# Kernel tuning notes

Measured on AMD Instinct MI355X. Metric: run time of the kernel, lower is better.

The kernel has to match this reference:

```python
import jax, jax.numpy as jnp
import numpy as np

N, E, D, L, B, T = 50000, 600000, 128, 7, 512, 10
ATOM_DIMS = [119, 4, 12, 12, 10, 6, 6, 2, 2]
BOND_DIMS = [5, 6, 2]
MSG_EPS = 1e-7   # GENConv message epsilon
BN_EPS = 1e-5    # torch BatchNorm1d eps


def _offsets(dims):
    return jnp.asarray(np.concatenate([[0], np.cumsum(dims[:-1])]), dtype=jnp.int32)


def setup_inputs():
    key = jax.random.key(0)
    k = lambda i: jax.random.fold_in(key, i)
    x = jnp.stack([jax.random.randint(k(i), (N,), 0, d) for i, d in enumerate(ATOM_DIMS)], axis=1)
    edge_attr = jnp.stack([jax.random.randint(k(100 + i), (E,), 0, d) for i, d in enumerate(BOND_DIMS)], axis=1)
    edge_index = jax.random.randint(k(200), (2, E), 0, N)
    batch = jnp.sort(jax.random.randint(k(201), (N,), 0, B))
    atom_table = 0.1 * jax.random.normal(k(300), (sum(ATOM_DIMS), D), jnp.float32)
    bond_table = 0.1 * jax.random.normal(k(301), (sum(BOND_DIMS), D), jnp.float32)
    norm_gamma = jnp.ones((L, D), jnp.float32)
    norm_beta = jnp.zeros((L, D), jnp.float32)
    t = 0.1 * jnp.ones((L,), jnp.float32)
    mlp_w1 = 0.05 * jax.random.normal(k(302), (L, D, 2 * D), jnp.float32)
    mlp_b1 = jnp.zeros((L, 2 * D), jnp.float32)
    mlp_bng = jnp.ones((L, 2 * D), jnp.float32)
    mlp_bnb = jnp.zeros((L, 2 * D), jnp.float32)
    mlp_w2 = 0.05 * jax.random.normal(k(303), (L, 2 * D, D), jnp.float32)
    mlp_b2 = jnp.zeros((L, D), jnp.float32)
    pred_w = 0.05 * jax.random.normal(k(304), (D, T), jnp.float32)
    pred_b = jnp.zeros((T,), jnp.float32)
    return dict(x=x, edge_index=edge_index, edge_attr=edge_attr, batch=batch,
                atom_offsets=_offsets(ATOM_DIMS), bond_offsets=_offsets(BOND_DIMS),
                atom_table=atom_table, bond_table=bond_table,
                norm_gamma=norm_gamma, norm_beta=norm_beta, t=t,
                mlp_w1=mlp_w1, mlp_b1=mlp_b1, mlp_bng=mlp_bng, mlp_bnb=mlp_bnb,
                mlp_w2=mlp_w2, mlp_b2=mlp_b2, pred_w=pred_w, pred_b=pred_b)


def _batchnorm(z, gamma, beta):
    # training-mode BatchNorm1d: batch stats, biased variance
    mu = z.mean(0)
    var = z.var(0)
    return (z - mu) * jax.lax.rsqrt(var + BN_EPS) * gamma + beta


def _genconv(h, ea, src, dst, t, w1, b1, g1, bt1, w2, b2):
    # GENConv: message = relu(x_j + edge_attr) + eps; softmax aggregation with temperature t
    msg = jax.nn.relu(h[src] + ea) + MSG_EPS                 # [E, D]
    logits = msg * t
    m = jax.ops.segment_max(logits, dst, num_segments=N)     # [N, D]
    m = jax.lax.stop_gradient(jnp.where(jnp.isfinite(m), m, 0.0))
    e = jnp.exp(logits - m[dst])
    denom = jax.ops.segment_sum(e, dst, num_segments=N)
    alpha = e / (denom[dst] + 1e-16)
    aggr = jax.ops.segment_sum(msg * alpha, dst, num_segments=N)  # [N, D]
    out = h + aggr                                           # update: x_r + aggr
    z = _batchnorm(out @ w1 + b1, g1, bt1)                   # MLP: D -> 2D (BN, ReLU) -> D
    return jax.nn.relu(z) @ w2 + b2


def reference(x, edge_index, edge_attr, batch, atom_offsets, bond_offsets,
              atom_table, bond_table, norm_gamma, norm_beta, t,
              mlp_w1, mlp_b1, mlp_bng, mlp_bnb, mlp_w2, mlp_b2, pred_w, pred_b):
    h = atom_table[x + atom_offsets[None, :]].sum(1)               # [N, D] AtomEncoder
    ea = bond_table[edge_attr + bond_offsets[None, :]].sum(1)      # [E, D] BondEncoder
    src, dst = edge_index[0], edge_index[1]
    # first layer: bare conv
    h = _genconv(h, ea, src, dst, t[0], mlp_w1[0], mlp_b1[0], mlp_bng[0], mlp_bnb[0], mlp_w2[0], mlp_b2[0])
    # remaining layers: res+ blocks (norm -> act -> conv -> residual); dropout=0
    for i in range(1, L):
        r = jax.nn.relu(_batchnorm(h, norm_gamma[i], norm_beta[i]))
        r = _genconv(r, ea, src, dst, t[i], mlp_w1[i], mlp_b1[i], mlp_bng[i], mlp_bnb[i], mlp_w2[i], mlp_b2[i])
        h = h + r
    h = _batchnorm(h, norm_gamma[0], norm_beta[0])                 # layers[0].norm
    # global mean pool over graphs
    sums = jax.ops.segment_sum(h, batch, num_segments=B)
    cnts = jax.ops.segment_sum(jnp.ones((N,), h.dtype), batch, num_segments=B)
    graph_emb = sums / jnp.maximum(cnts, 1.0)[:, None]
    return graph_emb @ pred_w + pred_b                             # [B, T]
```

## Files before the change

### kernel.cpp

```cpp
#include <hip/hip_runtime.h>
#include <hip/hip_bf16.h>

#define N_NODES 50000
#define N_EDGES 600000
#define D 128
#define D2 256
#define NGRAPH 512
#define NTARGET 10
#define NSB 49
#define NSLOT 32

static constexpr float MSG_EPS_F = 1e-7f;
static constexpr float BN_EPS_F  = 1e-5f;

typedef _Float16 half8 __attribute__((ext_vector_type(8)));
typedef _Float16 half4v __attribute__((ext_vector_type(4)));
typedef float f32x4 __attribute__((ext_vector_type(4)));
#define MFMA16(a, b, c) __builtin_amdgcn_mfma_f32_16x16x32_f16(a, b, c, 0, 0, 0)

__global__ __launch_bounds__(256) void k_encode(
    const int* __restrict__ x, const int* __restrict__ aoff,
    const float* __restrict__ atab, float* __restrict__ h,
    _Float16* __restrict__ rh, int* __restrict__ deg) {
  int tid = blockIdx.x * 256 + threadIdx.x;
  if (tid < N_NODES) deg[tid] = 0;
  int n = tid >> 5, f4 = (tid & 31) << 2;
  if (n >= N_NODES) return;
  float4 acc = make_float4(0.f, 0.f, 0.f, 0.f);
#pragma unroll
  for (int i = 0; i < 9; ++i) {
    int row = x[n * 9 + i] + aoff[i];
    float4 v = *(const float4*)&atab[row * D + f4];
    acc.x += v.x; acc.y += v.y; acc.z += v.z; acc.w += v.w;
  }
  *(float4*)&h[(size_t)n * D + f4] = acc;
  half4v o = {(_Float16)acc.x, (_Float16)acc.y, (_Float16)acc.z, (_Float16)acc.w};
  *(half4v*)&rh[(size_t)n * D + f4] = o;
}

__global__ __launch_bounds__(128) void k_combo(
    const int* __restrict__ boff, const float* __restrict__ btab,
    float* __restrict__ combo) {
  int c = blockIdx.x, t = threadIdx.x;
  int a0 = c / 12, a1 = (c % 12) / 2, a2 = c % 2;
  combo[c * D + t] = btab[(boff[0] + a0) * D + t] +
                     btab[(boff[1] + a1) * D + t] +
                     btab[(boff[2] + a2) * D + t];
}

__global__ __launch_bounds__(256) void k_packW(
    const float* __restrict__ w1, const float* __restrict__ w2,
    _Float16* __restrict__ w1p, _Float16* __restrict__ w2p) {
  int t = blockIdx.x * 256 + threadIdx.x;
  if (t < 7 * 4096) {
    int lane = t & 63, ntAll = (t >> 6) & 15, kc = (t >> 10) & 3, l = t >> 12;
    int q = lane >> 4, c = ntAll * 16 + (lane & 15);
    int kbase = kc * 32 + q * 8;
    const float* W = w1 + (size_t)l * D * D2;
    half8 v;
#pragma unroll
    for (int j = 0; j < 8; ++j) v[j] = (_Float16)W[(size_t)(kbase + j) * D2 + c];
    *(half8*)&w1p[(size_t)t * 8] = v;
  } else {
    int u = t - 7 * 4096;
    if (u < 7 * 4096) {
      int lane = u & 63, nt = (u >> 6) & 7, kcAll = (u >> 9) & 7, l = u >> 12;
      int q = lane >> 4, c = nt * 16 + (lane & 15);
      int kbase = kcAll * 32 + q * 8;
      const float* W = w2 + (size_t)l * D2 * D;
      half8 v;
#pragma unroll
      for (int j = 0; j < 8; ++j) v[j] = (_Float16)W[(size_t)(kbase + j) * D + c];
      *(half8*)&w2p[(size_t)u * 8] = v;
    }
  }
}

__global__ __launch_bounds__(256) void k_degree(
    const int* __restrict__ ei, int* __restrict__ deg) {
  int e = blockIdx.x * 256 + threadIdx.x;
  if (e >= N_EDGES) return;
  atomicAdd(&deg[ei[N_EDGES + e]], 1);
}

__global__ __launch_bounds__(1024) void k_scan1(
    const int* __restrict__ deg, int* __restrict__ excl, int* __restrict__ bsum) {
  __shared__ int tmp[1024];
  int t = threadIdx.x, i = blockIdx.x * 1024 + t;
  int v = (i < N_NODES) ? deg[i] : 0;
  tmp[t] = v;
  __syncthreads();
  for (int off = 1; off < 1024; off <<= 1) {
    int add = (t >= off) ? tmp[t - off] : 0;
    __syncthreads();
    tmp[t] += add;
    __syncthreads();
  }
  if (i < N_NODES) excl[i] = tmp[t] - v;
  if (t == 1023) bsum[blockIdx.x] = tmp[1023];
}

__global__ __launch_bounds__(64) void k_scan2(int* __restrict__ bsum) {
  __shared__ int s[64];
  int t = threadIdx.x;
  int v = (t < NSB) ? bsum[t] : 0;
  s[t] = v;
  __syncthreads();
  for (int off = 1; off < 64; off <<= 1) {
    int add = (t >= off) ? s[t - off] : 0;
    __syncthreads();
    s[t] += add;
    __syncthreads();
  }
  if (t < NSB) bsum[t] = s[t] - v;
}

__global__ __launch_bounds__(256) void k_scan3(
    const int* __restrict__ excl, const int* __restrict__ bsum,
    int* __restrict__ rowptr, int* __restrict__ cursor) {
  int i = blockIdx.x * 256 + threadIdx.x;
  if (i < N_NODES) {
    int v = excl[i] + bsum[i >> 10];
    rowptr[i] = v;
    cursor[i] = v;
  }
  if (i == N_NODES) rowptr[N_NODES] = N_EDGES;
}

__global__ __launch_bounds__(256) void k_scatter(
    const int* __restrict__ ei, const int* __restrict__ eattr,
    int* __restrict__ cursor, int* __restrict__ payload) {
  int e = blockIdx.x * 256 + threadIdx.x;
  if (e >= N_EDGES) return;
  int src = ei[e], dst = ei[N_EDGES + e];
  int cid = eattr[e * 3 + 0] * 12 + eattr[e * 3 + 1] * 2 + eattr[e * 3 + 2];
  int pos = atomicAdd(&cursor[dst], 1);
  payload[pos] = (src << 6) | cid;
}

__global__ __launch_bounds__(256) void k_gbounds(
    const int* __restrict__ batch, int* __restrict__ gstart) {
  int n = blockIdx.x * 256 + threadIdx.x;
  if (n >= N_NODES) return;
  int b0 = batch[n];
  int b1 = (n + 1 < N_NODES) ? batch[n + 1] : NGRAPH;
  for (int bb = b0 + 1; bb <= b1; ++bb) gstart[bb] = n + 1;
  if (n == 0)
    for (int bb = 0; bb <= b0; ++bb) gstart[bb] = 0;
}

__global__ __launch_bounds__(256) void k_prenorm(
    const float* __restrict__ h, const float* __restrict__ statHs,
    const float* __restrict__ gamma, const float* __restrict__ beta,
    _Float16* __restrict__ rh) {
  __shared__ float sH[256];
  int t = threadIdx.x;
  {
    float a = 0.f;
#pragma unroll
    for (int s = 0; s < NSLOT; ++s) a += statHs[s * 256 + t];
    sH[t] = a;
  }
  __syncthreads();
  int tid = blockIdx.x * 256 + t;
  int n = tid >> 5, f4 = (t & 31) << 2;
  if (n >= N_NODES) return;
  const float invN = 1.0f / (float)N_NODES;
  float4 s  = *(const float4*)&sH[f4];
  float4 sq = *(const float4*)&sH[D + f4];
  float4 g  = *(const float4*)&gamma[f4];
  float4 b  = *(const float4*)&beta[f4];
  float4 hv = *(const float4*)&h[(size_t)n * D + f4];
  float mu = s.x * invN, var = sq.x * invN - mu * mu;
  float ox = fmaxf((hv.x - mu) * rsqrtf(var + BN_EPS_F) * g.x + b.x, 0.f);
  mu = s.y * invN; var = sq.y * invN - mu * mu;
  float oy = fmaxf((hv.y - mu) * rsqrtf(var + BN_EPS_F) * g.y + b.y, 0.f);
  mu = s.z * invN; var = sq.z * invN - mu * mu;
  float oz = fmaxf((hv.z - mu) * rsqrtf(var + BN_EPS_F) * g.z + b.z, 0.f);
  mu = s.w * invN; var = sq.w * invN - mu * mu;
  float ow = fmaxf((hv.w - mu) * rsqrtf(var + BN_EPS_F) * g.w + b.w, 0.f);
  half4v o = {(_Float16)ox, (_Float16)oy, (_Float16)oz, (_Float16)ow};
  *(half4v*)&rh[(size_t)n * D + f4] = o;
}

__global__ __launch_bounds__(256) void k_aggr(
    const _Float16* __restrict__ rh, const int* __restrict__ rowptr,
    const int* __restrict__ payload, const float* __restrict__ combo,
    const float* __restrict__ tptr, int l, _Float16* __restrict__ aggrh,
    float* __restrict__ stat1s, float* __restrict__ statHs) {
  if (blockIdx.x < NSLOT) {
    float* z1 = stat1s + blockIdx.x * 512;
    float* zH = statHs + blockIdx.x * 256;
    for (int j = threadIdx.x; j < 768; j += 256) {
      if (j < 512) z1[j] = 0.f;
      else zH[j - 512] = 0.f;
    }
  }
  int tid = blockIdx.x * 256 + threadIdx.x;
  int dst = tid >> 5, f4 = (tid & 31) << 2;
  if (dst >= N_NODES) return;
  float tv = tptr[l];
  int s = rowptr[dst], e = rowptr[dst + 1];
  float4 den = make_float4(0.f, 0.f, 0.f, 0.f);
  float4 S = make_float4(0.f, 0.f, 0.f, 0.f);
  int i = s;
  for (; i + 1 < e; i += 2) {
    int p0 = payload[i], p1 = payload[i + 1];
    half4v r0 = *(const half4v*)&rh[(size_t)(p0 >> 6) * D + f4];
    half4v r1 = *(const half4v*)&rh[(size_t)(p1 >> 6) * D + f4];
    float4 cv0 = *(const float4*)&combo[(p0 & 63) * D + f4];
    float4 cv1 = *(const float4*)&combo[(p1 & 63) * D + f4];
    float m0x = fmaxf((float)r0[0] + cv0.x, 0.f) + MSG_EPS_F;
    float m0y = fmaxf((float)r0[1] + cv0.y, 0.f) + MSG_EPS_F;
    float m0z = fmaxf((float)r0[2] + cv0.z, 0.f) + MSG_EPS_F;
    float m0w = fmaxf((float)r0[3] + cv0.w, 0.f) + MSG_EPS_F;
    float m1x = fmaxf((float)r1[0] + cv1.x, 0.f) + MSG_EPS_F;
    float m1y = fmaxf((float)r1[1] + cv1.y, 0.f) + MSG_EPS_F;
    float m1z = fmaxf((float)r1[2] + cv1.z, 0.f) + MSG_EPS_F;
    float m1w = fmaxf((float)r1[3] + cv1.w, 0.f) + MSG_EPS_F;
    float e0x = __expf(m0x * tv), e0y = __expf(m0y * tv);
    float e0z = __expf(m0z * tv), e0w = __expf(m0w * tv);
    float e1x = __expf(m1x * tv), e1y = __expf(m1y * tv);
    float e1z = __expf(m1z * tv), e1w = __expf(m1w * tv);
    den.x += e0x + e1x; den.y += e0y + e1y;
    den.z += e0z + e1z; den.w += e0w + e1w;
    S.x += m0x * e0x + m1x * e1x; S.y += m0y * e0y + m1y * e1y;
    S.z += m0z * e0z + m1z * e1z; S.w += m0w * e0w + m1w * e1w;
  }
  if (i < e) {
    int p0 = payload[i];
    half4v r0 = *(const half4v*)&rh[(size_t)(p0 >> 6) * D + f4];
    float4 cv0 = *(const float4*)&combo[(p0 & 63) * D + f4];
    float m0x = fmaxf((float)r0[0] + cv0.x, 0.f) + MSG_EPS_F;
    float m0y = fmaxf((float)r0[1] + cv0.y, 0.f) + MSG_EPS_F;
    float m0z = fmaxf((float)r0[2] + cv0.z, 0.f) + MSG_EPS_F;
    float m0w = fmaxf((float)r0[3] + cv0.w, 0.f) + MSG_EPS_F;
    float e0x = __expf(m0x * tv), e0y = __expf(m0y * tv);
    float e0z = __expf(m0z * tv), e0w = __expf(m0w * tv);
    den.x += e0x; den.y += e0y; den.z += e0z; den.w += e0w;
    S.x += m0x * e0x; S.y += m0y * e0y; S.z += m0z * e0z; S.w += m0w * e0w;
  }
  half4v o;
  o[0] = (_Float16)(S.x / (den.x + 1e-16f));
  o[1] = (_Float16)(S.y / (den.y + 1e-16f));
  o[2] = (_Float16)(S.z / (den.z + 1e-16f));
  o[3] = (_Float16)(S.w / (den.w + 1e-16f));
  *(half4v*)&aggrh[(size_t)dst * D + f4] = o;
}

__global__ __launch_bounds__(256) void k_gemm1(
    const _Float16* __restrict__ rh, const _Float16* __restrict__ aggrh,
    const _Float16* __restrict__ w1p, const float* __restrict__ b1,
    _Float16* __restrict__ z1h, float* __restrict__ stat1s) {
  __shared__ __align__(16) _Float16 Af[512 * 8];
  int tid = threadIdx.x;
  int row0 = blockIdx.x * 32;
  int slot = blockIdx.x & (NSLOT - 1);

#pragma unroll
  for (int s0 = 0; s0 < 2; ++s0) {
    int s = s0 * 256 + tid;
    int kc = s >> 7, mt = (s >> 6) & 1, l2 = s & 63;
    int row = row0 + mt * 16 + (l2 & 15);
    int kb = kc * 32 + ((l2 >> 4) << 3);
    half8 v;
    if (row < N_NODES) {
      half8 rv = *(const half8*)&rh[(size_t)row * D + kb];
      half8 av = *(const half8*)&aggrh[(size_t)row * D + kb];
      v = rv + av;
    } else {
#pragma unroll
      for (int j = 0; j < 8; ++j) v[j] = (_Float16)0.f;
    }
    *(half8*)&Af[s * 8] = v;
  }
  __syncthreads();

  int wv = tid >> 6, ln = tid & 63;
  f32x4 acc[2][4];
#pragma unroll
  for (int i = 0; i < 2; ++i)
#pragma unroll
    for (int j = 0; j < 4; ++j) acc[i][j] = (f32x4){0.f, 0.f, 0.f, 0.f};

#pragma unroll
  for (int kc = 0; kc < 4; ++kc) {
    half8 a0 = *(half8*)&Af[((kc * 2 + 0) * 64 + ln) * 8];
    half8 a1 = *(half8*)&Af[((kc * 2 + 1) * 64 + ln) * 8];
#pragma unroll
    for (int nt = 0; nt < 4; ++nt) {
      int ntAll = wv * 4 + nt;
      half8 b = *(const half8*)&w1p[((size_t)(kc * 16 + ntAll) * 64 + ln) * 8];
      acc[0][nt] = MFMA16(a0, b, acc[0][nt]);
      acc[1][nt] = MFMA16(a1, b, acc[1][nt]);
    }
  }
  int lq = ln >> 4, lc = ln & 15;
  float cs[4], cq[4];
#pragma unroll
  for (int nt = 0; nt < 4; ++nt) { cs[nt] = 0.f; cq[nt] = 0.f; }
#pragma unroll
  for (int nt = 0; nt < 4; ++nt) {
    int col = (wv * 4 + nt) * 16 + lc;
    float bias = b1[col];
#pragma unroll
    for (int mt = 0; mt < 2; ++mt) {
      int rbase = row0 + mt * 16 + lq * 4;
#pragma unroll
      for (int rg = 0; rg < 4; ++rg) {
        int row = rbase + rg;
        if (row < N_NODES) {
          float z = acc[mt][nt][rg] + bias;
          z1h[(size_t)row * D2 + col] = (_Float16)z;
          cs[nt] += z; cq[nt] += z * z;
        }
      }
    }
  }
#pragma unroll
  for (int nt = 0; nt < 4; ++nt) {
    float v = cs[nt], q = cq[nt];
    v += __shfl_xor(v, 16); v += __shfl_xor(v, 32);
    q += __shfl_xor(q, 16); q += __shfl_xor(q, 32);
    if (lq == 0) {
      int col = (wv * 4 + nt) * 16 + lc;
      atomicAdd(&stat1s[slot * 512 + col], v);
      atomicAdd(&stat1s[slot * 512 + 256 + col], q);
    }
  }
}

__global__ __launch_bounds__(256) void k_gemm2(
    const _Float16* __restrict__ z1h, const float* __restrict__ stat1s,
    const float* __restrict__ g1, const float* __restrict__ bt1,
    const _Float16* __restrict__ w2p, const float* __restrict__ b2,
    float* __restrict__ h, int residual, float* __restrict__ statHs) {
  __shared__ __align__(16) _Float16 Af[1024 * 8];
  __shared__ float s1[512];
  const float invN = 1.0f / (float)N_NODES;
  int tid = threadIdx.x;
  int row0 = blockIdx.x * 32;
  int slot = blockIdx.x & (NSLOT - 1);

#pragma unroll
  for (int jj = 0; jj < 2; ++jj) {
    int j = jj * 256 + tid;
    float a = 0.f;
#pragma unroll
    for (int s = 0; s < NSLOT; ++s) a += stat1s[s * 512 + j];
    s1[j] = a;
  }
  __syncthreads();

#pragma unroll
  for (int s0 = 0; s0 < 4; ++s0) {
    int s = s0 * 256 + tid;
    int kcAll = s >> 7, mt = (s >> 6) & 1, l2 = s & 63;
    int row = row0 + mt * 16 + (l2 & 15);
    int kb = kcAll * 32 + ((l2 >> 4) << 3);
    half8 v;
    if (row < N_NODES) {
      half8 z = *(const half8*)&z1h[(size_t)row * D2 + kb];
#pragma unroll
      for (int j = 0; j < 8; ++j) {
        float mu = s1[kb + j] * invN;
        float isg = rsqrtf(s1[256 + kb + j] * invN - mu * mu + BN_EPS_F) * g1[kb + j];
        v[j] = (_Float16)fmaxf(((float)z[j] - mu) * isg + bt1[kb + j], 0.f);
      }
    } else {
#pragma unroll
      for (int j = 0; j < 8; ++j) v[j] = (_Float16)0.f;
    }
    *(half8*)&Af[s * 8] = v;
  }
  __syncthreads();

  int wv = tid >> 6, ln = tid & 63;
  f32x4 acc[2][2];
#pragma unroll
  for (int i = 0; i < 2; ++i)
#pragma unroll
    for (int j = 0; j < 2; ++j) acc[i][j] = (f32x4){0.f, 0.f, 0.f, 0.f};

#pragma unroll
  for (int kcAll = 0; kcAll < 8; ++kcAll) {
    half8 a0 = *(half8*)&Af[((kcAll * 2 + 0) * 64 + ln) * 8];
    half8 a1 = *(half8*)&Af[((kcAll * 2 + 1) * 64 + ln) * 8];
#pragma unroll
    for (int nt = 0; nt < 2; ++nt) {
      half8 b = *(const half8*)&w2p[((size_t)(kcAll * 8 + wv * 2 + nt) * 64 + ln) * 8];
      acc[0][nt] = MFMA16(a0, b, acc[0][nt]);
      acc[1][nt] = MFMA16(a1, b, acc[1][nt]);
    }
  }
  int lq = ln >> 4, lc = ln & 15;
  float cs[2], cq[2];
#pragma unroll
  for (int nt = 0; nt < 2; ++nt) { cs[nt] = 0.f; cq[nt] = 0.f; }
#pragma unroll
  for (int nt = 0; nt < 2; ++nt) {
    int col = (wv * 2 + nt) * 16 + lc;
    float bias = b2[col];
#pragma unroll
    for (int mt = 0; mt < 2; ++mt) {
      int rbase = row0 + mt * 16 + lq * 4;
#pragma unroll
      for (int rg = 0; rg < 4; ++rg) {
        int row = rbase + rg;
        if (row < N_NODES) {
          float v = acc[mt][nt][rg] + bias;
          if (residual) v += h[(size_t)row * D + col];
          h[(size_t)row * D + col] = v;
          cs[nt] += v; cq[nt] += v * v;
        }
      }
    }
  }
#pragma unroll
  for (int nt = 0; nt < 2; ++nt) {
    float v = cs[nt], q = cq[nt];
    v += __shfl_xor(v, 16); v += __shfl_xor(v, 32);
    q += __shfl_xor(q, 16); q += __shfl_xor(q, 32);
    if (lq == 0) {
      int col = (wv * 2 + nt) * 16 + lc;
      atomicAdd(&statHs[slot * 256 + col], v);
      atomicAdd(&statHs[slot * 256 + 128 + col], q);
    }
  }
}

__global__ __launch_bounds__(256) void k_pool(
    const float* __restrict__ h, const int* __restrict__ gstart,
    float* __restrict__ psum) {
  __shared__ float4 red[256];
  int b = blockIdx.x, tid = threadIdx.x;
  int fl = (tid & 31) << 2, ns = tid >> 5;
  int gs = gstart[b], ge = gstart[b + 1];
  float4 acc = make_float4(0.f, 0.f, 0.f, 0.f);
  for (int n = gs + ns; n < ge; n += 8) {
    float4 v = *(const float4*)&h[(size_t)n * D + fl];
    acc.x += v.x; acc.y += v.y; acc.z += v.z; acc.w += v.w;
  }
  red[tid] = acc;
  __syncthreads();
  if (ns < 4) {
    float4 o = red[tid + 128];
    acc.x += o.x; acc.y += o.y; acc.z += o.z; acc.w += o.w;
    red[tid] = acc;
  }
  __syncthreads();
  if (ns < 2) {
    float4 o = red[tid + 64];
    acc.x += o.x; acc.y += o.y; acc.z += o.z; acc.w += o.w;
    red[tid] = acc;
  }
  __syncthreads();
  if (ns == 0) {
    float4 o = red[tid + 32];
    acc.x += o.x; acc.y += o.y; acc.z += o.z; acc.w += o.w;
    *(float4*)&psum[(size_t)b * D + fl] = acc;
  }
}

__global__ __launch_bounds__(64) void k_pred(
    const float* __restrict__ psum, const int* __restrict__ gstart,
    const float* __restrict__ statHs, const float* __restrict__ gamma,
    const float* __restrict__ beta, const float* __restrict__ pw,
    const float* __restrict__ pb, float* __restrict__ out) {
  __shared__ float sH[256];
  int b = blockIdx.x, t = threadIdx.x;
  for (int j = t; j < 256; j += 64) {
    float a = 0.f;
#pragma unroll
    for (int s = 0; s < NSLOT; ++s) a += statHs[s * 256 + j];
    sH[j] = a;
  }
  __syncthreads();
  if (t >= NTARGET) return;
  int gs = gstart[b], ge = gstart[b + 1];
  float acc = pb[t];
  if (ge > gs) {
    const float invN = 1.0f / (float)N_NODES;
    float inv = 1.0f / (float)(ge - gs);
    for (int k = 0; k < D; ++k) {
      float mu = sH[k] * invN;
      float var = sH[D + k] * invN - mu * mu;
      float emb = (psum[(size_t)b * D + k] * inv - mu) * rsqrtf(var + BN_EPS_F) * gamma[k] + beta[k];
      acc += emb * pw[k * NTARGET + t];
    }
  }
  out[b * NTARGET + t] = acc;
}

extern "C" void kernel_launch(void* const* d_in, const int* in_sizes, int n_in,
                              void* d_out, int out_size, void* d_ws, size_t ws_size,
                              hipStream_t stream) {
  const int* x      = (const int*)d_in[0];
  const int* ei     = (const int*)d_in[1];
  const int* eattr  = (const int*)d_in[2];
  const int* batch  = (const int*)d_in[3];
  const int* aoff   = (const int*)d_in[4];
  const int* boff   = (const int*)d_in[5];
  const float* atab = (const float*)d_in[6];
  const float* btab = (const float*)d_in[7];
  const float* ngam = (const float*)d_in[8];
  const float* nbet = (const float*)d_in[9];
  const float* tptr = (const float*)d_in[10];
  const float* w1   = (const float*)d_in[11];
  const float* b1   = (const float*)d_in[12];
  const float* bng  = (const float*)d_in[13];
  const float* bnb  = (const float*)d_in[14];
  const float* w2   = (const float*)d_in[15];
  const float* b2   = (const float*)d_in[16];
  const float* pw   = (const float*)d_in[17];
  const float* pb   = (const float*)d_in[18];
  float* out = (float*)d_out;

  float* ws = (float*)d_ws;
  const size_t ND = (size_t)N_NODES * D;
  float* h      = ws;
  _Float16* rh  = (_Float16*)(ws + 1 * ND);
  _Float16* aggrh = (_Float16*)(ws + 1 * ND + ND / 2);
  _Float16* z1h = (_Float16*)(ws + 2 * ND);
  float* stat1s = ws + 3 * ND;
  float* statHs = stat1s + NSLOT * 512;
  float* psum   = statHs + NSLOT * 256;
  float* combo  = psum + (size_t)NGRAPH * D;
  _Float16* w1p = (_Float16*)(combo + 60 * D);
  _Float16* w2p = w1p + 7 * 32768;
  int* ibuf     = (int*)(w2p + 7 * 32768);
  int* rowptr   = ibuf;
  int* cursor   = rowptr + N_NODES + 1;
  int* deg      = cursor + N_NODES;
  int* payload  = deg + N_NODES;
  int* gstart   = payload + N_EDGES;
  int* excl     = gstart + NGRAPH + 1;
  int* bsum     = excl + N_NODES;

  const int nodeBlocks = (N_NODES * 32 + 255) / 256;
  const int edgeThreadBlocks = (N_EDGES + 255) / 256;
  const int nBlocks256 = (N_NODES + 255) / 256;
  const int gRows32 = (N_NODES + 31) / 32;

  k_encode<<<nodeBlocks, 256, 0, stream>>>(x, aoff, atab, h, rh, deg);
  k_combo<<<60, 128, 0, stream>>>(boff, btab, combo);
  k_packW<<<(2 * 7 * 4096 + 255) / 256, 256, 0, stream>>>(w1, w2, w1p, w2p);
  k_gbounds<<<nBlocks256, 256, 0, stream>>>(batch, gstart);
  k_degree<<<edgeThreadBlocks, 256, 0, stream>>>(ei, deg);
  k_scan1<<<NSB, 1024, 0, stream>>>(deg, excl, bsum);
  k_scan2<<<1, 64, 0, stream>>>(bsum);
  k_scan3<<<(N_NODES + 256) / 256, 256, 0, stream>>>(excl, bsum, rowptr, cursor);
  k_scatter<<<edgeThreadBlocks, 256, 0, stream>>>(ei, eattr, cursor, payload);

  for (int l = 0; l < 7; ++l) {
    if (l > 0)
      k_prenorm<<<nodeBlocks, 256, 0, stream>>>(h, statHs, ngam + l * D, nbet + l * D, rh);
    k_aggr<<<nodeBlocks, 256, 0, stream>>>(rh, rowptr, payload, combo, tptr, l, aggrh,
                                           stat1s, statHs);
    k_gemm1<<<gRows32, 256, 0, stream>>>(rh, aggrh, w1p + (size_t)l * 32768,
                                         b1 + l * D2, z1h, stat1s);
    k_gemm2<<<gRows32, 256, 0, stream>>>(z1h, stat1s, bng + l * D2, bnb + l * D2,
                                         w2p + (size_t)l * 32768, b2 + l * D,
                                         h, l > 0 ? 1 : 0, statHs);
  }

  k_pool<<<NGRAPH, 256, 0, stream>>>(h, gstart, psum);
  k_pred<<<NGRAPH, 64, 0, stream>>>(psum, gstart, statHs, ngam, nbet, pw, pb, out);
}
```

Measured before the change: 909.3 us.

## Widen aggregation lanes, store combo in fp16, fuse residual add and pool/pred

The aggregation kernel now gives each thread 8 features through half8 loads, using 16 threads per node instead of 32, and reads the bond-combo table in fp16. It adds the node's own features to the aggregate before writing, so gemm1 reads one fp16 input instead of two. The pool and prediction kernels are merged into one launch. Together these cut gather bandwidth, gemm1 input traffic and launch count, at the price of fp16 rounding of the combo table and fewer threads per node in aggregation.

```diff
diff --git a/kernel.cpp b/kernel.cpp
--- a/kernel.cpp
+++ b/kernel.cpp
@@ -40,12 +40,12 @@
 
 __global__ __launch_bounds__(128) void k_combo(
     const int* __restrict__ boff, const float* __restrict__ btab,
-    float* __restrict__ combo) {
+    _Float16* __restrict__ comboh) {
   int c = blockIdx.x, t = threadIdx.x;
   int a0 = c / 12, a1 = (c % 12) / 2, a2 = c % 2;
-  combo[c * D + t] = btab[(boff[0] + a0) * D + t] +
-                     btab[(boff[1] + a1) * D + t] +
-                     btab[(boff[2] + a2) * D + t];
+  comboh[c * D + t] = (_Float16)(btab[(boff[0] + a0) * D + t] +
+                                 btab[(boff[1] + a1) * D + t] +
+                                 btab[(boff[2] + a2) * D + t]);
 }
 
 __global__ __launch_bounds__(256) void k_packW(
@@ -185,8 +185,8 @@
 
 __global__ __launch_bounds__(256) void k_aggr(
     const _Float16* __restrict__ rh, const int* __restrict__ rowptr,
-    const int* __restrict__ payload, const float* __restrict__ combo,
-    const float* __restrict__ tptr, int l, _Float16* __restrict__ aggrh,
+    const int* __restrict__ payload, const _Float16* __restrict__ comboh,
+    const float* __restrict__ tptr, int l, _Float16* __restrict__ xh,
     float* __restrict__ stat1s, float* __restrict__ statHs) {
   if (blockIdx.x < NSLOT) {
     float* z1 = stat1s + blockIdx.x * 512;
@@ -197,61 +197,53 @@
     }
   }
   int tid = blockIdx.x * 256 + threadIdx.x;
-  int dst = tid >> 5, f4 = (tid & 31) << 2;
+  int dst = tid >> 4, f8 = (tid & 15) << 3;
   if (dst >= N_NODES) return;
   float tv = tptr[l];
   int s = rowptr[dst], e = rowptr[dst + 1];
-  float4 den = make_float4(0.f, 0.f, 0.f, 0.f);
-  float4 S = make_float4(0.f, 0.f, 0.f, 0.f);
+  float den[8], S[8];
+#pragma unroll
+  for (int j = 0; j < 8; ++j) { den[j] = 0.f; S[j] = 0.f; }
   int i = s;
   for (; i + 1 < e; i += 2) {
     int p0 = payload[i], p1 = payload[i + 1];
-    half4v r0 = *(const half4v*)&rh[(size_t)(p0 >> 6) * D + f4];
-    half4v r1 = *(const half4v*)&rh[(size_t)(p1 >> 6) * D + f4];
-    float4 cv0 = *(const float4*)&combo[(p0 & 63) * D + f4];
-    float4 cv1 = *(const float4*)&combo[(p1 & 63) * D + f4];
-    float m0x = fmaxf((float)r0[0] + cv0.x, 0.f) + MSG_EPS_F;
-    float m0y = fmaxf((float)r0[1] + cv0.y, 0.f) + MSG_EPS_F;
-    float m0z = fmaxf((float)r0[2] + cv0.z, 0.f) + MSG_EPS_F;
-    float m0w = fmaxf((float)r0[3] + cv0.w, 0.f) + MSG_EPS_F;
-    float m1x = fmaxf((float)r1[0] + cv1.x, 0.f) + MSG_EPS_F;
-    float m1y = fmaxf((float)r1[1] + cv1.y, 0.f) + MSG_EPS_F;
-    float m1z = fmaxf((float)r1[2] + cv1.z, 0.f) + MSG_EPS_F;
-    float m1w = fmaxf((float)r1[3] + cv1.w, 0.f) + MSG_EPS_F;
-    float e0x = __expf(m0x * tv), e0y = __expf(m0y * tv);
-    float e0z = __expf(m0z * tv), e0w = __expf(m0w * tv);
-    float e1x = __expf(m1x * tv), e1y = __expf(m1y * tv);
-    float e1z = __expf(m1z * tv), e1w = __expf(m1w * tv);
-    den.x += e0x + e1x; den.y += e0y + e1y;
-    den.z += e0z + e1z; den.w += e0w + e1w;
-    S.x += m0x * e0x + m1x * e1x; S.y += m0y * e0y + m1y * e1y;
-    S.z += m0z * e0z + m1z * e1z; S.w += m0w * e0w + m1w * e1w;
+    half8 r0 = *(const half8*)&rh[(size_t)(p0 >> 6) * D + f8];
+    half8 r1 = *(const half8*)&rh[(size_t)(p1 >> 6) * D + f8];
+    half8 c0 = *(const half8*)&comboh[(p0 & 63) * D + f8];
+    half8 c1 = *(const half8*)&comboh[(p1 & 63) * D + f8];
+#pragma unroll
+    for (int j = 0; j < 8; ++j) {
+      float m0 = fmaxf((float)r0[j] + (float)c0[j], 0.f) + MSG_EPS_F;
+      float m1 = fmaxf((float)r1[j] + (float)c1[j], 0.f) + MSG_EPS_F;
+      float e0 = __expf(m0 * tv), e1 = __expf(m1 * tv);
+      den[j] += e0 + e1;
+      S[j] += m0 * e0 + m1 * e1;
+    }
   }
   if (i < e) {
     int p0 = payload[i];
-    half4v r0 = *(const half4v*)&rh[(size_t)(p0 >> 6) * D + f4];
-    float4 cv0 = *(const float4*)&combo[(p0 & 63) * D + f4];
-    float m0x = fmaxf((float)r0[0] + cv0.x, 0.f) + MSG_EPS_F;
-    float m0y = fmaxf((float)r0[1] + cv0.y, 0.f) + MSG_EPS_F;
-    float m0z = fmaxf((float)r0[2] + cv0.z, 0.f) + MSG_EPS_F;
-    float m0w = fmaxf((float)r0[3] + cv0.w, 0.f) + MSG_EPS_F;
-    float e0x = __expf(m0x * tv), e0y = __expf(m0y * tv);
-    float e0z = __expf(m0z * tv), e0w = __expf(m0w * tv);
-    den.x += e0x; den.y += e0y; den.z += e0z; den.w += e0w;
-    S.x += m0x * e0x; S.y += m0y * e0y; S.z += m0z * e0z; S.w += m0w * e0w;
-  }
-  half4v o;
-  o[0] = (_Float16)(S.x / (den.x + 1e-16f));
-  o[1] = (_Float16)(S.y / (den.y + 1e-16f));
-  o[2] = (_Float16)(S.z / (den.z + 1e-16f));
-  o[3] = (_Float16)(S.w / (den.w + 1e-16f));
-  *(half4v*)&aggrh[(size_t)dst * D + f4] = o;
+    half8 r0 = *(const half8*)&rh[(size_t)(p0 >> 6) * D + f8];
+    half8 c0 = *(const half8*)&comboh[(p0 & 63) * D + f8];
+#pragma unroll
+    for (int j = 0; j < 8; ++j) {
+      float m0 = fmaxf((float)r0[j] + (float)c0[j], 0.f) + MSG_EPS_F;
+      float e0 = __expf(m0 * tv);
+      den[j] += e0;
+      S[j] += m0 * e0;
+    }
+  }
+  half8 ro = *(const half8*)&rh[(size_t)dst * D + f8];
+  half8 o;
+#pragma unroll
+  for (int j = 0; j < 8; ++j)
+    o[j] = (_Float16)((float)ro[j] + S[j] / (den[j] + 1e-16f));
+  *(half8*)&xh[(size_t)dst * D + f8] = o;
 }
 
 __global__ __launch_bounds__(256) void k_gemm1(
-    const _Float16* __restrict__ rh, const _Float16* __restrict__ aggrh,
-    const _Float16* __restrict__ w1p, const float* __restrict__ b1,
-    _Float16* __restrict__ z1h, float* __restrict__ stat1s) {
+    const _Float16* __restrict__ xh, const _Float16* __restrict__ w1p,
+    const float* __restrict__ b1, _Float16* __restrict__ z1h,
+    float* __restrict__ stat1s) {
   __shared__ __align__(16) _Float16 Af[512 * 8];
   int tid = threadIdx.x;
   int row0 = blockIdx.x * 32;
@@ -265,9 +257,7 @@
     int kb = kc * 32 + ((l2 >> 4) << 3);
     half8 v;
     if (row < N_NODES) {
-      half8 rv = *(const half8*)&rh[(size_t)row * D + kb];
-      half8 av = *(const half8*)&aggrh[(size_t)row * D + kb];
-      v = rv + av;
+      v = *(const half8*)&xh[(size_t)row * D + kb];
     } else {
 #pragma unroll
       for (int j = 0; j < 8; ++j) v[j] = (_Float16)0.f;
@@ -429,11 +419,21 @@
   }
 }
 
-__global__ __launch_bounds__(256) void k_pool(
+__global__ __launch_bounds__(256) void k_poolpred(
     const float* __restrict__ h, const int* __restrict__ gstart,
-    float* __restrict__ psum) {
+    const float* __restrict__ statHs, const float* __restrict__ gamma,
+    const float* __restrict__ beta, const float* __restrict__ pw,
+    const float* __restrict__ pb, float* __restrict__ out) {
+  __shared__ float sH[256];
+  __shared__ float emb[128];
   __shared__ float4 red[256];
   int b = blockIdx.x, tid = threadIdx.x;
+  {
+    float a = 0.f;
+#pragma unroll
+    for (int s = 0; s < NSLOT; ++s) a += statHs[s * 256 + tid];
+    sH[tid] = a;
+  }
   int fl = (tid & 31) << 2, ns = tid >> 5;
   int gs = gstart[b], ge = gstart[b + 1];
   float4 acc = make_float4(0.f, 0.f, 0.f, 0.f);
@@ -458,38 +458,25 @@
   if (ns == 0) {
     float4 o = red[tid + 32];
     acc.x += o.x; acc.y += o.y; acc.z += o.z; acc.w += o.w;
-    *(float4*)&psum[(size_t)b * D + fl] = acc;
-  }
-}
-
-__global__ __launch_bounds__(64) void k_pred(
-    const float* __restrict__ psum, const int* __restrict__ gstart,
-    const float* __restrict__ statHs, const float* __restrict__ gamma,
-    const float* __restrict__ beta, const float* __restrict__ pw,
-    const float* __restrict__ pb, float* __restrict__ out) {
-  __shared__ float sH[256];
-  int b = blockIdx.x, t = threadIdx.x;
-  for (int j = t; j < 256; j += 64) {
-    float a = 0.f;
-#pragma unroll
-    for (int s = 0; s < NSLOT; ++s) a += statHs[s * 256 + j];
-    sH[j] = a;
-  }
-  __syncthreads();
-  if (t >= NTARGET) return;
-  int gs = gstart[b], ge = gstart[b + 1];
-  float acc = pb[t];
-  if (ge > gs) {
     const float invN = 1.0f / (float)N_NODES;
-    float inv = 1.0f / (float)(ge - gs);
-    for (int k = 0; k < D; ++k) {
+    float inv = (ge > gs) ? 1.0f / (float)(ge - gs) : 0.f;
+    float av[4] = {acc.x, acc.y, acc.z, acc.w};
+#pragma unroll
+    for (int j = 0; j < 4; ++j) {
+      int k = fl + j;
       float mu = sH[k] * invN;
       float var = sH[D + k] * invN - mu * mu;
-      float emb = (psum[(size_t)b * D + k] * inv - mu) * rsqrtf(var + BN_EPS_F) * gamma[k] + beta[k];
-      acc += emb * pw[k * NTARGET + t];
-    }
-  }
-  out[b * NTARGET + t] = acc;
+      emb[k] = (ge > gs)
+          ? (av[j] * inv - mu) * rsqrtf(var + BN_EPS_F) * gamma[k] + beta[k]
+          : 0.f;
+    }
+  }
+  __syncthreads();
+  if (tid < NTARGET) {
+    float o = pb[tid];
+    for (int k = 0; k < D; ++k) o += emb[k] * pw[k * NTARGET + tid];
+    out[b * NTARGET + tid] = o;
+  }
 }
 
 extern "C" void kernel_launch(void* const* d_in, const int* in_sizes, int n_in,
@@ -520,13 +507,14 @@
   const size_t ND = (size_t)N_NODES * D;
   float* h      = ws;
   _Float16* rh  = (_Float16*)(ws + 1 * ND);
-  _Float16* aggrh = (_Float16*)(ws + 1 * ND + ND / 2);
+  _Float16* xh  = (_Float16*)(ws + 1 * ND + ND / 2);
   _Float16* z1h = (_Float16*)(ws + 2 * ND);
   float* stat1s = ws + 3 * ND;
   float* statHs = stat1s + NSLOT * 512;
   float* psum   = statHs + NSLOT * 256;
-  float* combo  = psum + (size_t)NGRAPH * D;
-  _Float16* w1p = (_Float16*)(combo + 60 * D);
+  float* comboF = psum + (size_t)NGRAPH * D;
+  _Float16* comboh = (_Float16*)comboF;
+  _Float16* w1p = (_Float16*)(comboF + 60 * D);
   _Float16* w2p = w1p + 7 * 32768;
   int* ibuf     = (int*)(w2p + 7 * 32768);
   int* rowptr   = ibuf;
@@ -538,12 +526,13 @@
   int* bsum     = excl + N_NODES;
 
   const int nodeBlocks = (N_NODES * 32 + 255) / 256;
+  const int aggrBlocks = (N_NODES * 16 + 255) / 256;
   const int edgeThreadBlocks = (N_EDGES + 255) / 256;
   const int nBlocks256 = (N_NODES + 255) / 256;
   const int gRows32 = (N_NODES + 31) / 32;
 
   k_encode<<<nodeBlocks, 256, 0, stream>>>(x, aoff, atab, h, rh, deg);
-  k_combo<<<60, 128, 0, stream>>>(boff, btab, combo);
+  k_combo<<<60, 128, 0, stream>>>(boff, btab, comboh);
   k_packW<<<(2 * 7 * 4096 + 255) / 256, 256, 0, stream>>>(w1, w2, w1p, w2p);
   k_gbounds<<<nBlocks256, 256, 0, stream>>>(batch, gstart);
   k_degree<<<edgeThreadBlocks, 256, 0, stream>>>(ei, deg);
@@ -555,15 +544,14 @@
   for (int l = 0; l < 7; ++l) {
     if (l > 0)
       k_prenorm<<<nodeBlocks, 256, 0, stream>>>(h, statHs, ngam + l * D, nbet + l * D, rh);
-    k_aggr<<<nodeBlocks, 256, 0, stream>>>(rh, rowptr, payload, combo, tptr, l, aggrh,
+    k_aggr<<<aggrBlocks, 256, 0, stream>>>(rh, rowptr, payload, comboh, tptr, l, xh,
                                            stat1s, statHs);
-    k_gemm1<<<gRows32, 256, 0, stream>>>(rh, aggrh, w1p + (size_t)l * 32768,
+    k_gemm1<<<gRows32, 256, 0, stream>>>(xh, w1p + (size_t)l * 32768,
                                          b1 + l * D2, z1h, stat1s);
     k_gemm2<<<gRows32, 256, 0, stream>>>(z1h, stat1s, bng + l * D2, bnb + l * D2,
                                          w2p + (size_t)l * 32768, b2 + l * D,
                                          h, l > 0 ? 1 : 0, statHs);
   }
 
-  k_pool<<<NGRAPH, 256, 0, stream>>>(h, gstart, psum);
-  k_pred<<<NGRAPH, 64, 0, stream>>>(psum, gstart, statHs, ngam, nbet, pw, pb, out);
-}
+  k_poolpred<<<NGRAPH, 256, 0, stream>>>(h, gstart, statHs, ngam, nbet, pw, pb, out);
+}
```

New measurement: 909.7 us. Within noise of the previous version (+0.1%).
